# Kernel optimization log

Measured on AMD Instinct MI355X. Metric: run time of the kernel, lower is better.

## Reference

```python
import jax, jax.numpy as jnp
import numpy as np

NUM_HEADS = 16
HEAD_DIM = 64  # att_output_dim // num_heads = 1024 // 16


def setup_inputs() -> dict:
    key = jax.random.key(0)
    ks = jax.random.split(key, 7)
    B, S, D_IN, D_OUT = 4, 2048, 1024, 1024
    std = 1.0 / np.sqrt(D_IN)
    return {
        "ts10_input": jax.random.normal(ks[0], (B, S, D_IN), dtype=jnp.float32),
        "Wq": jax.random.uniform(ks[1], (D_IN, D_OUT), jnp.float32, -std, std),
        "bq": jax.random.uniform(ks[2], (D_OUT,), jnp.float32, -std, std),
        "Wk": jax.random.uniform(ks[3], (D_IN, D_OUT), jnp.float32, -std, std),
        "bk": jax.random.uniform(ks[4], (D_OUT,), jnp.float32, -std, std),
        "Wv": jax.random.uniform(ks[5], (D_IN, D_OUT), jnp.float32, -std, std),
        "bv": jax.random.uniform(ks[6], (D_OUT,), jnp.float32, -std, std),
        "mask": 1,
    }


def reference(ts10_input, Wq, bq, Wk, bk, Wv, bv, mask):
    B, S, _ = ts10_input.shape
    H, Dh = NUM_HEADS, HEAD_DIM

    def split_heads(x):  # (B,S,H*Dh) -> (B,H,S,Dh)
        return x.reshape(B, S, H, Dh).transpose(0, 2, 1, 3)

    q = split_heads(ts10_input @ Wq + bq)
    k = split_heads(ts10_input @ Wk + bk)
    v = split_heads(ts10_input @ Wv + bv)

    scores = jnp.einsum("bhqd,bhkd->bhqk", q, k) / jnp.sqrt(jnp.float32(Dh))
    if mask:
        causal = jnp.tril(jnp.ones((S, S), dtype=bool))  # keep lower triangle incl diag
        scores = jnp.where(causal, scores, -jnp.inf)
    probs = jax.nn.softmax(scores, axis=-1)
    ctx = jnp.einsum("bhqk,bhkd->bhqd", probs, v)
    return ctx.transpose(0, 2, 1, 3).reshape(B, S, H * Dh)
```

## Files before the change

kernel.cpp:

```cpp
#include <hip/hip_runtime.h>

typedef __bf16 bf16x8 __attribute__((ext_vector_type(8)));
typedef __bf16 bf16x4 __attribute__((ext_vector_type(4)));
typedef short s16x4 __attribute__((ext_vector_type(4)));
typedef float f32x4 __attribute__((ext_vector_type(4)));
typedef unsigned short u16x8 __attribute__((ext_vector_type(8)));
typedef unsigned short u16x4 __attribute__((ext_vector_type(4)));
typedef unsigned int u32x2 __attribute__((ext_vector_type(2)));
typedef unsigned int __attribute__((address_space(1))) as1_uint;
typedef unsigned int __attribute__((address_space(3))) as3_uint;

#define S_LEN 2048
#define NB 4
#define NH 16
#define HD 64
#define DM 1024

#define Q_SCALE 0.18033688011112042f

__device__ __forceinline__ unsigned short f2bf(float f) {
  union { float f; unsigned int u; } v; v.f = f;
  unsigned int r = v.u + 0x7fffu + ((v.u >> 16) & 1u);
  return (unsigned short)(r >> 16);
}

__device__ __forceinline__ unsigned int fbits(float f) {
  union { float f; unsigned int u; } v; v.f = f;
  return v.u;
}

__device__ __forceinline__ f32x4 mfma16(u16x4 a, u16x4 b, f32x4 c) {
#if __has_builtin(__builtin_amdgcn_mfma_f32_16x16x16_bf16)
  return __builtin_amdgcn_mfma_f32_16x16x16_bf16(
      __builtin_bit_cast(bf16x4, a), __builtin_bit_cast(bf16x4, b), c, 0, 0, 0);
#else
  return __builtin_amdgcn_mfma_f32_16x16x16bf16_1k(
      __builtin_bit_cast(s16x4, a), __builtin_bit_cast(s16x4, b), c, 0, 0, 0);
#endif
}

__global__ __launch_bounds__(256) void cvt_x(const float* __restrict__ x,
                                             unsigned short* __restrict__ xb) {
  int i = (blockIdx.x * 256 + threadIdx.x) * 8;
  f32x4 a = *(const f32x4*)(x + i);
  f32x4 b = *(const f32x4*)(x + i + 4);
  u16x8 o;
  o[0] = f2bf(a[0]); o[1] = f2bf(a[1]); o[2] = f2bf(a[2]); o[3] = f2bf(a[3]);
  o[4] = f2bf(b[0]); o[5] = f2bf(b[1]); o[6] = f2bf(b[2]); o[7] = f2bf(b[3]);
  *(u16x8*)(xb + i) = o;
}

__global__ __launch_bounds__(256) void cvt_wt(const float* __restrict__ Wq,
                                              const float* __restrict__ Wk,
                                              const float* __restrict__ Wv,
                                              unsigned short* __restrict__ wt) {
  const float* W = (blockIdx.z == 0) ? Wq : (blockIdx.z == 1) ? Wk : Wv;
  unsigned short* WT = wt + (size_t)blockIdx.z * DM * DM;
  __shared__ float tile[32][33];
  int tx = threadIdx.x & 31, ty = threadIdx.x >> 5;
  int k0 = blockIdx.x * 32, n0 = blockIdx.y * 32;
#pragma unroll
  for (int i = 0; i < 4; ++i)
    tile[ty + 8 * i][tx] = W[(size_t)(k0 + ty + 8 * i) * DM + n0 + tx];
  __syncthreads();
#pragma unroll
  for (int i = 0; i < 4; ++i)
    WT[(size_t)(n0 + ty + 8 * i) * DM + k0 + tx] = f2bf(tile[tx][ty + 8 * i]);
}

#define QKV_LDS_BYTES 147456
__global__ __launch_bounds__(512, 2) void qkv_gemm(const unsigned short* __restrict__ xb,
                                                   const unsigned short* __restrict__ wt,
                                                   const float* __restrict__ bq,
                                                   const float* __restrict__ bk,
                                                   const float* __restrict__ bv,
                                                   unsigned short* __restrict__ qo,
                                                   unsigned short* __restrict__ ko,
                                                   unsigned short* __restrict__ vto) {
  extern __shared__ char smem_dyn[];
  unsigned short* As = (unsigned short*)smem_dyn;
  unsigned short* Bs = As + 3 * 256 * 64;
  const int z = blockIdx.z;
  const unsigned short* WT = wt + (size_t)z * DM * DM;
  const float* bias = (z == 0) ? bq : (z == 1) ? bk : bv;
  const int m0 = blockIdx.x * 256;
  const int n0 = blockIdx.y * 128;
  const int tid = threadIdx.x;
  const int wave = tid >> 6, lane = tid & 63, quad = lane >> 4, lw = lane & 15;
  const int wm = (wave >> 1) * 64, wn = (wave & 1) * 64;

  f32x4 acc[4][4];
#pragma unroll
  for (int mt = 0; mt < 4; ++mt)
#pragma unroll
    for (int nt = 0; nt < 4; ++nt) acc[mt][nt] = (f32x4){0.f, 0.f, 0.f, 0.f};

  auto stage = [&](int tile) {
    const int kt = tile * 64;
    const int bsel = tile % 3;
    unsigned short* Ad = As + bsel * (256 * 64);
    unsigned short* Bd = Bs + bsel * (128 * 64);
#pragma unroll
    for (int i = 0; i < 4; ++i) {
      int c = i * 512 + tid;
      int row = c >> 3, scn = (c & 7) ^ (row & 7);
      __builtin_amdgcn_global_load_lds((const as1_uint*)(xb + (size_t)(m0 + row) * DM + kt + scn * 8),
                                       (as3_uint*)(Ad + c * 8), 16, 0, 0);
    }
#pragma unroll
    for (int i = 0; i < 2; ++i) {
      int c = i * 512 + tid;
      int row = c >> 3, scn = (c & 7) ^ (row & 7);
      __builtin_amdgcn_global_load_lds((const as1_uint*)(WT + (size_t)(n0 + row) * DM + kt + scn * 8),
                                       (as3_uint*)(Bd + c * 8), 16, 0, 0);
    }
  };

  stage(0);
  stage(1);
  asm volatile("s_waitcnt vmcnt(6)" ::: "memory");
  __builtin_amdgcn_s_barrier();
  asm volatile("" ::: "memory");

#pragma unroll
  for (int t = 0; t < 16; ++t) {
    if (t + 2 < 16) stage(t + 2);

    const unsigned short* Ab = As + (t % 3) * (256 * 64);
    const unsigned short* Bb = Bs + (t % 3) * (128 * 64);
    bf16x8 af[2][4], bfq[2][4];
#pragma unroll
    for (int k = 0; k < 2; ++k) {
#pragma unroll
      for (int mt = 0; mt < 4; ++mt) {
        int r = wm + mt * 16 + lw;
        af[k][mt] = *(const bf16x8*)(Ab + r * 64 + (((k * 4 + quad) ^ (r & 7)) * 8));
      }
#pragma unroll
      for (int nt = 0; nt < 4; ++nt) {
        int r = wn + nt * 16 + lw;
        bfq[k][nt] = *(const bf16x8*)(Bb + r * 64 + (((k * 4 + quad) ^ (r & 7)) * 8));
      }
    }
#pragma unroll
    for (int k = 0; k < 2; ++k)
#pragma unroll
      for (int mt = 0; mt < 4; ++mt)
#pragma unroll
        for (int nt = 0; nt < 4; ++nt)
          acc[mt][nt] = __builtin_amdgcn_mfma_f32_16x16x32_bf16(af[k][mt], bfq[k][nt], acc[mt][nt], 0, 0, 0);

    if (t < 15) {
      if (t < 14) asm volatile("s_waitcnt vmcnt(6)" ::: "memory");
      else        asm volatile("s_waitcnt vmcnt(0)" ::: "memory");
      __builtin_amdgcn_s_barrier();
      asm volatile("" ::: "memory");
    }
  }

  float bias4[4];
#pragma unroll
  for (int nt = 0; nt < 4; ++nt) bias4[nt] = bias[n0 + wn + nt * 16 + lw];

  if (z < 2) {
    unsigned short* dst = (z == 0) ? qo : ko;
    const float sc = (z == 0) ? Q_SCALE : 1.0f;
#pragma unroll
    for (int mt = 0; mt < 4; ++mt) {
#pragma unroll
      for (int nt = 0; nt < 4; ++nt) {
        int n = n0 + wn + nt * 16 + lw;
        int h = n >> 6, d = n & 63;
#pragma unroll
        for (int r = 0; r < 4; ++r) {
          int m = m0 + wm + mt * 16 + quad * 4 + r;
          int b = m >> 11, s = m & 2047;
          dst[((size_t)(b * NH + h) * S_LEN + s) * HD + d] = f2bf((acc[mt][nt][r] + bias4[nt]) * sc);
        }
      }
    }
  } else {
#pragma unroll
    for (int mt = 0; mt < 4; ++mt) {
#pragma unroll
      for (int nt = 0; nt < 4; ++nt) {
        int n = n0 + wn + nt * 16 + lw;
        int h = n >> 6, d = n & 63;
        int mb = m0 + wm + mt * 16 + quad * 4;
        int b = mb >> 11, s = mb & 2047;
        u16x4 pk;
#pragma unroll
        for (int r = 0; r < 4; ++r) pk[r] = f2bf(acc[mt][nt][r] + bias4[nt]);
        *(u16x4*)(vto + ((size_t)(b * NH + h) * HD + d) * S_LEN + s) = pk;
      }
    }
  }
}

__global__ __launch_bounds__(256, 4) void attn(const unsigned short* __restrict__ Qb,
                                               const unsigned short* __restrict__ Kb,
                                               const unsigned short* __restrict__ Vtb,
                                               float* __restrict__ out) {
  const int flat = blockIdx.x;
  const int bh_lo = flat & 7;
  const int qpair = (flat >> 3) & 15;
  const int bh_hi = flat >> 7;
  const int bh = bh_lo + 8 * bh_hi;
  const int b = bh >> 4, h = bh & 15;
  const int tid = threadIdx.x;
  const int wave = tid >> 6, lane = tid & 63;
  const int quad = lane >> 4, lw = lane & 15;
  const int qlo = qpair * 64;
  const int qhi = (31 - qpair) * 64;
  const unsigned short* Qp = Qb + (size_t)bh * S_LEN * HD;
  const unsigned short* Kp = Kb + (size_t)bh * S_LEN * HD;
  const unsigned short* Vp = Vtb + (size_t)bh * HD * S_LEN;

  __shared__ __align__(16) unsigned short Kl[2][64 * 64];
  __shared__ __align__(16) unsigned short Vl[2][64 * 64];

  bf16x8 aq[2][2];
#pragma unroll
  for (int rg = 0; rg < 2; ++rg) {
    const int qbase = rg ? qhi : qlo;
#pragma unroll
    for (int kc = 0; kc < 2; ++kc)
      aq[rg][kc] = *(const bf16x8*)(Qp + (size_t)(qbase + wave * 16 + lw) * HD + kc * 32 + quad * 8);
  }

  u16x4 ones4;
#pragma unroll
  for (int i = 0; i < 4; ++i) ones4[i] = 0x3F80;

  f32x4 accO[2][4];
  f32x4 accL[2];
#pragma unroll
  for (int rg = 0; rg < 2; ++rg) {
    accL[rg] = (f32x4){0.f, 0.f, 0.f, 0.f};
#pragma unroll
    for (int dg = 0; dg < 4; ++dg) accO[rg][dg] = (f32x4){0.f, 0.f, 0.f, 0.f};
  }

  const int qr0 = qlo + wave * 16 + lw;
  const int qr1 = qhi + wave * 16 + lw;

  const int T = 32 - qpair;

  {
#pragma unroll
    for (int i = 0; i < 2; ++i) {
      int idx = i * 256 + tid;
      int r = idx >> 3, c = (idx & 7) ^ (r & 7);
      __builtin_amdgcn_global_load_lds((const as1_uint*)(Kp + (size_t)r * HD + c * 8),
                                       (as3_uint*)(Kl[0] + idx * 8), 16, 0, 0);
      __builtin_amdgcn_global_load_lds((const as1_uint*)(Vp + (size_t)r * S_LEN + c * 8),
                                       (as3_uint*)(Vl[0] + idx * 8), 16, 0, 0);
    }
  }

  for (int t = 0; t < T; ++t) {
    const int kv = t * 64;
    const int cur = t & 1;
    __syncthreads();

    if (t + 1 < T) {
      const int kvn = kv + 64;
#pragma unroll
      for (int i = 0; i < 2; ++i) {
        int idx = i * 256 + tid;
        int r = idx >> 3, c = (idx & 7) ^ (r & 7);
        __builtin_amdgcn_global_load_lds((const as1_uint*)(Kp + (size_t)(kvn + r) * HD + c * 8),
                                         (as3_uint*)(Kl[cur ^ 1] + idx * 8), 16, 0, 0);
        __builtin_amdgcn_global_load_lds((const as1_uint*)(Vp + (size_t)r * S_LEN + kvn + c * 8),
                                         (as3_uint*)(Vl[cur ^ 1] + idx * 8), 16, 0, 0);
      }
    }

    const bool a0 = (t <= qpair);
    const bool d0 = (t == qpair);
    const bool d1 = (t == T - 1);

#pragma unroll
    for (int g = 0; g < 4; ++g) {
      const unsigned short* kp = Kl[cur] + (g * 16 + lw) * 64;
      const int sw = lw & 7;
      bf16x8 kf0 = *(const bf16x8*)(kp + ((quad ^ sw) * 8));
      bf16x8 kf1 = *(const bf16x8*)(kp + (((4 + quad) ^ sw) * 8));

      u16x4 pf[2];
#pragma unroll
      for (int rg = 0; rg < 2; ++rg) {
        if (rg == 0 && !a0) continue;
        f32x4 s = (f32x4){0.f, 0.f, 0.f, 0.f};
        s = __builtin_amdgcn_mfma_f32_16x16x32_bf16(kf0, aq[rg][0], s, 0, 0, 0);
        s = __builtin_amdgcn_mfma_f32_16x16x32_bf16(kf1, aq[rg][1], s, 0, 0, 0);
        const bool dg_ = rg ? d1 : d0;
        const int qr = rg ? qr1 : qr0;
        if (dg_) {
#pragma unroll
          for (int r = 0; r < 4; ++r) {
            float e = __builtin_amdgcn_exp2f(s[r]);
            s[r] = (kv + g * 16 + quad * 4 + r > qr) ? 0.f : e;
          }
        } else {
#pragma unroll
          for (int r = 0; r < 4; ++r) s[r] = __builtin_amdgcn_exp2f(s[r]);
        }
        u32x2 pk;
        pk[0] = (fbits(s[1]) & 0xFFFF0000u) | (fbits(s[0]) >> 16);
        pk[1] = (fbits(s[3]) & 0xFFFF0000u) | (fbits(s[2]) >> 16);
        pf[rg] = __builtin_bit_cast(u16x4, pk);
      }

#pragma unroll
      for (int dg = 0; dg < 4; ++dg) {
        const int row = dg * 16 + lw;
        const int slot = (2 * g + (quad >> 1)) ^ (lw & 7);
        u16x4 vf = *(const u16x4*)(Vl[cur] + row * 64 + slot * 8 + (quad & 1) * 4);
        if (a0) accO[0][dg] = mfma16(pf[0], vf, accO[0][dg]);
        accO[1][dg] = mfma16(pf[1], vf, accO[1][dg]);
      }
      if (a0) accL[0] = mfma16(pf[0], ones4, accL[0]);
      accL[1] = mfma16(pf[1], ones4, accL[1]);
    }
  }

#pragma unroll
  for (int rg = 0; rg < 2; ++rg) {
    const int qbase = rg ? qhi : qlo;
    float* op = out + ((size_t)b * S_LEN + qbase + wave * 16 + quad * 4) * DM + h * HD + lw;
#pragma unroll
    for (int r = 0; r < 4; ++r) {
      float inv = 1.0f / accL[rg][r];
#pragma unroll
      for (int dg = 0; dg < 4; ++dg) op[(size_t)r * DM + dg * 16] = accO[rg][dg][r] * inv;
    }
  }
}

extern "C" void kernel_launch(void* const* d_in, const int* in_sizes, int n_in,
                              void* d_out, int out_size, void* d_ws, size_t ws_size,
                              hipStream_t stream) {
  const float* x = (const float*)d_in[0];
  const float* Wq = (const float*)d_in[1];
  const float* bq = (const float*)d_in[2];
  const float* Wk = (const float*)d_in[3];
  const float* bk = (const float*)d_in[4];
  const float* Wv = (const float*)d_in[5];
  const float* bv = (const float*)d_in[6];
  float* out = (float*)d_out;

  char* ws = (char*)d_ws;
  unsigned short* xb = (unsigned short*)(ws + 0);
  unsigned short* wt = (unsigned short*)(ws + 16777216);
  unsigned short* qb = (unsigned short*)(ws + 23068672);
  unsigned short* kb = (unsigned short*)(ws + 39845888);
  unsigned short* vt = (unsigned short*)(ws + 56623104);

  hipFuncSetAttribute((const void*)qkv_gemm,
                      hipFuncAttributeMaxDynamicSharedMemorySize, QKV_LDS_BYTES);

  hipLaunchKernelGGL(cvt_x, dim3(4096), dim3(256), 0, stream, x, xb);
  hipLaunchKernelGGL(cvt_wt, dim3(32, 32, 3), dim3(256), 0, stream, Wq, Wk, Wv, wt);
  hipLaunchKernelGGL(qkv_gemm, dim3(32, 8, 3), dim3(512), QKV_LDS_BYTES, stream,
                     xb, wt, bq, bk, bv, qb, kb, vt);
  hipLaunchKernelGGL(attn, dim3(1024), dim3(256), 0, stream, qb, kb, vt, out);
}
```

Baseline: 221.9 us.

## Split attention into one q-tile per block, read V directly, fuse convert kernels

Merges the x and weight conversion kernels into a single launch, which removes one kernel launch. The attention kernel no longer pairs low and high query tiles. It now runs one 64-row query tile per block, with 2048 blocks ordered longest-first and occupancy raised to 6. V is no longer staged through LDS and is read directly from global memory per MFMA, which halves the LDS footprint. A setprio hint is added around the compute. The uncoalesced strided global V reads and the loss of the paired load balancing could offset the gains from higher occupancy.

```diff
diff --git a/kernel.cpp b/kernel.cpp
--- a/kernel.cpp
+++ b/kernel.cpp
@@ -39,33 +39,38 @@
 #endif
 }
 
-__global__ __launch_bounds__(256) void cvt_x(const float* __restrict__ x,
-                                             unsigned short* __restrict__ xb) {
-  int i = (blockIdx.x * 256 + threadIdx.x) * 8;
-  f32x4 a = *(const f32x4*)(x + i);
-  f32x4 b = *(const f32x4*)(x + i + 4);
-  u16x8 o;
-  o[0] = f2bf(a[0]); o[1] = f2bf(a[1]); o[2] = f2bf(a[2]); o[3] = f2bf(a[3]);
-  o[4] = f2bf(b[0]); o[5] = f2bf(b[1]); o[6] = f2bf(b[2]); o[7] = f2bf(b[3]);
-  *(u16x8*)(xb + i) = o;
-}
-
-__global__ __launch_bounds__(256) void cvt_wt(const float* __restrict__ Wq,
-                                              const float* __restrict__ Wk,
-                                              const float* __restrict__ Wv,
-                                              unsigned short* __restrict__ wt) {
-  const float* W = (blockIdx.z == 0) ? Wq : (blockIdx.z == 1) ? Wk : Wv;
-  unsigned short* WT = wt + (size_t)blockIdx.z * DM * DM;
+__global__ __launch_bounds__(256) void cvt_all(const float* __restrict__ x,
+                                               unsigned short* __restrict__ xb,
+                                               const float* __restrict__ Wq,
+                                               const float* __restrict__ Wk,
+                                               const float* __restrict__ Wv,
+                                               unsigned short* __restrict__ wt) {
   __shared__ float tile[32][33];
-  int tx = threadIdx.x & 31, ty = threadIdx.x >> 5;
-  int k0 = blockIdx.x * 32, n0 = blockIdx.y * 32;
-#pragma unroll
-  for (int i = 0; i < 4; ++i)
-    tile[ty + 8 * i][tx] = W[(size_t)(k0 + ty + 8 * i) * DM + n0 + tx];
-  __syncthreads();
-#pragma unroll
-  for (int i = 0; i < 4; ++i)
-    WT[(size_t)(n0 + ty + 8 * i) * DM + k0 + tx] = f2bf(tile[tx][ty + 8 * i]);
+  const int bid = blockIdx.x;
+  if (bid < 4096) {
+    int i = (bid * 256 + threadIdx.x) * 8;
+    f32x4 a = *(const f32x4*)(x + i);
+    f32x4 b = *(const f32x4*)(x + i + 4);
+    u16x8 o;
+    o[0] = f2bf(a[0]); o[1] = f2bf(a[1]); o[2] = f2bf(a[2]); o[3] = f2bf(a[3]);
+    o[4] = f2bf(b[0]); o[5] = f2bf(b[1]); o[6] = f2bf(b[2]); o[7] = f2bf(b[3]);
+    *(u16x8*)(xb + i) = o;
+  } else {
+    const int r = bid - 4096;
+    const int z = r >> 10;
+    const int rr = r & 1023;
+    const float* W = (z == 0) ? Wq : (z == 1) ? Wk : Wv;
+    unsigned short* WT = wt + (size_t)z * DM * DM;
+    int tx = threadIdx.x & 31, ty = threadIdx.x >> 5;
+    int k0 = (rr & 31) * 32, n0 = (rr >> 5) * 32;
+#pragma unroll
+    for (int i = 0; i < 4; ++i)
+      tile[ty + 8 * i][tx] = W[(size_t)(k0 + ty + 8 * i) * DM + n0 + tx];
+    __syncthreads();
+#pragma unroll
+    for (int i = 0; i < 4; ++i)
+      WT[(size_t)(n0 + ty + 8 * i) * DM + k0 + tx] = f2bf(tile[tx][ty + 8 * i]);
+  }
 }
 
 #define QKV_LDS_BYTES 147456
@@ -197,65 +202,50 @@
   }
 }
 
-__global__ __launch_bounds__(256, 4) void attn(const unsigned short* __restrict__ Qb,
+__global__ __launch_bounds__(256, 6) void attn(const unsigned short* __restrict__ Qb,
                                                const unsigned short* __restrict__ Kb,
                                                const unsigned short* __restrict__ Vtb,
                                                float* __restrict__ out) {
   const int flat = blockIdx.x;
   const int bh_lo = flat & 7;
-  const int qpair = (flat >> 3) & 15;
-  const int bh_hi = flat >> 7;
-  const int bh = bh_lo + 8 * bh_hi;
+  const int rest = flat >> 3;
+  const int qidx = 31 - (rest >> 3);
+  const int bh_hi = rest & 7;
+  const int bh = bh_lo | (bh_hi << 3);
   const int b = bh >> 4, h = bh & 15;
   const int tid = threadIdx.x;
   const int wave = tid >> 6, lane = tid & 63;
   const int quad = lane >> 4, lw = lane & 15;
-  const int qlo = qpair * 64;
-  const int qhi = (31 - qpair) * 64;
   const unsigned short* Qp = Qb + (size_t)bh * S_LEN * HD;
   const unsigned short* Kp = Kb + (size_t)bh * S_LEN * HD;
   const unsigned short* Vp = Vtb + (size_t)bh * HD * S_LEN;
 
   __shared__ __align__(16) unsigned short Kl[2][64 * 64];
-  __shared__ __align__(16) unsigned short Vl[2][64 * 64];
-
-  bf16x8 aq[2][2];
-#pragma unroll
-  for (int rg = 0; rg < 2; ++rg) {
-    const int qbase = rg ? qhi : qlo;
-#pragma unroll
-    for (int kc = 0; kc < 2; ++kc)
-      aq[rg][kc] = *(const bf16x8*)(Qp + (size_t)(qbase + wave * 16 + lw) * HD + kc * 32 + quad * 8);
-  }
+
+  const int qbase = qidx * 64;
+  bf16x8 aq[2];
+#pragma unroll
+  for (int kc = 0; kc < 2; ++kc)
+    aq[kc] = *(const bf16x8*)(Qp + (size_t)(qbase + wave * 16 + lw) * HD + kc * 32 + quad * 8);
 
   u16x4 ones4;
 #pragma unroll
   for (int i = 0; i < 4; ++i) ones4[i] = 0x3F80;
 
-  f32x4 accO[2][4];
-  f32x4 accL[2];
-#pragma unroll
-  for (int rg = 0; rg < 2; ++rg) {
-    accL[rg] = (f32x4){0.f, 0.f, 0.f, 0.f};
-#pragma unroll
-    for (int dg = 0; dg < 4; ++dg) accO[rg][dg] = (f32x4){0.f, 0.f, 0.f, 0.f};
-  }
-
-  const int qr0 = qlo + wave * 16 + lw;
-  const int qr1 = qhi + wave * 16 + lw;
-
-  const int T = 32 - qpair;
-
-  {
-#pragma unroll
-    for (int i = 0; i < 2; ++i) {
-      int idx = i * 256 + tid;
-      int r = idx >> 3, c = (idx & 7) ^ (r & 7);
-      __builtin_amdgcn_global_load_lds((const as1_uint*)(Kp + (size_t)r * HD + c * 8),
-                                       (as3_uint*)(Kl[0] + idx * 8), 16, 0, 0);
-      __builtin_amdgcn_global_load_lds((const as1_uint*)(Vp + (size_t)r * S_LEN + c * 8),
-                                       (as3_uint*)(Vl[0] + idx * 8), 16, 0, 0);
-    }
+  f32x4 accO[4];
+  f32x4 accL = (f32x4){0.f, 0.f, 0.f, 0.f};
+#pragma unroll
+  for (int dg = 0; dg < 4; ++dg) accO[dg] = (f32x4){0.f, 0.f, 0.f, 0.f};
+
+  const int qr = qbase + wave * 16 + lw;
+  const int T = qidx + 1;
+
+#pragma unroll
+  for (int i = 0; i < 2; ++i) {
+    int idx = i * 256 + tid;
+    int r = idx >> 3, c = (idx & 7) ^ (r & 7);
+    __builtin_amdgcn_global_load_lds((const as1_uint*)(Kp + (size_t)r * HD + c * 8),
+                                     (as3_uint*)(Kl[0] + idx * 8), 16, 0, 0);
   }
 
   for (int t = 0; t < T; ++t) {
@@ -271,15 +261,11 @@
         int r = idx >> 3, c = (idx & 7) ^ (r & 7);
         __builtin_amdgcn_global_load_lds((const as1_uint*)(Kp + (size_t)(kvn + r) * HD + c * 8),
                                          (as3_uint*)(Kl[cur ^ 1] + idx * 8), 16, 0, 0);
-        __builtin_amdgcn_global_load_lds((const as1_uint*)(Vp + (size_t)r * S_LEN + kvn + c * 8),
-                                         (as3_uint*)(Vl[cur ^ 1] + idx * 8), 16, 0, 0);
-      }
-    }
-
-    const bool a0 = (t <= qpair);
-    const bool d0 = (t == qpair);
-    const bool d1 = (t == T - 1);
-
+      }
+    }
+
+    const bool diag = (t == qidx);
+    __builtin_amdgcn_s_setprio(1);
 #pragma unroll
     for (int g = 0; g < 4; ++g) {
       const unsigned short* kp = Kl[cur] + (g * 16 + lw) * 64;
@@ -287,54 +273,41 @@
       bf16x8 kf0 = *(const bf16x8*)(kp + ((quad ^ sw) * 8));
       bf16x8 kf1 = *(const bf16x8*)(kp + (((4 + quad) ^ sw) * 8));
 
-      u16x4 pf[2];
-#pragma unroll
-      for (int rg = 0; rg < 2; ++rg) {
-        if (rg == 0 && !a0) continue;
-        f32x4 s = (f32x4){0.f, 0.f, 0.f, 0.f};
-        s = __builtin_amdgcn_mfma_f32_16x16x32_bf16(kf0, aq[rg][0], s, 0, 0, 0);
-        s = __builtin_amdgcn_mfma_f32_16x16x32_bf16(kf1, aq[rg][1], s, 0, 0, 0);
-        const bool dg_ = rg ? d1 : d0;
-        const int qr = rg ? qr1 : qr0;
-        if (dg_) {
-#pragma unroll
-          for (int r = 0; r < 4; ++r) {
-            float e = __builtin_amdgcn_exp2f(s[r]);
-            s[r] = (kv + g * 16 + quad * 4 + r > qr) ? 0.f : e;
-          }
-        } else {
-#pragma unroll
-          for (int r = 0; r < 4; ++r) s[r] = __builtin_amdgcn_exp2f(s[r]);
+      f32x4 s = (f32x4){0.f, 0.f, 0.f, 0.f};
+      s = __builtin_amdgcn_mfma_f32_16x16x32_bf16(kf0, aq[0], s, 0, 0, 0);
+      s = __builtin_amdgcn_mfma_f32_16x16x32_bf16(kf1, aq[1], s, 0, 0, 0);
+      if (diag) {
+#pragma unroll
+        for (int r = 0; r < 4; ++r) {
+          float e = __builtin_amdgcn_exp2f(s[r]);
+          s[r] = (kv + g * 16 + quad * 4 + r > qr) ? 0.f : e;
         }
-        u32x2 pk;
-        pk[0] = (fbits(s[1]) & 0xFFFF0000u) | (fbits(s[0]) >> 16);
-        pk[1] = (fbits(s[3]) & 0xFFFF0000u) | (fbits(s[2]) >> 16);
-        pf[rg] = __builtin_bit_cast(u16x4, pk);
-      }
-
+      } else {
+#pragma unroll
+        for (int r = 0; r < 4; ++r) s[r] = __builtin_amdgcn_exp2f(s[r]);
+      }
+      u32x2 pk;
+      pk[0] = (fbits(s[1]) & 0xFFFF0000u) | (fbits(s[0]) >> 16);
+      pk[1] = (fbits(s[3]) & 0xFFFF0000u) | (fbits(s[2]) >> 16);
+      u16x4 pf = __builtin_bit_cast(u16x4, pk);
+
+      const unsigned short* vg = Vp + (size_t)lw * S_LEN + kv + g * 16 + quad * 4;
 #pragma unroll
       for (int dg = 0; dg < 4; ++dg) {
-        const int row = dg * 16 + lw;
-        const int slot = (2 * g + (quad >> 1)) ^ (lw & 7);
-        u16x4 vf = *(const u16x4*)(Vl[cur] + row * 64 + slot * 8 + (quad & 1) * 4);
-        if (a0) accO[0][dg] = mfma16(pf[0], vf, accO[0][dg]);
-        accO[1][dg] = mfma16(pf[1], vf, accO[1][dg]);
-      }
-      if (a0) accL[0] = mfma16(pf[0], ones4, accL[0]);
-      accL[1] = mfma16(pf[1], ones4, accL[1]);
-    }
-  }
-
-#pragma unroll
-  for (int rg = 0; rg < 2; ++rg) {
-    const int qbase = rg ? qhi : qlo;
-    float* op = out + ((size_t)b * S_LEN + qbase + wave * 16 + quad * 4) * DM + h * HD + lw;
-#pragma unroll
-    for (int r = 0; r < 4; ++r) {
-      float inv = 1.0f / accL[rg][r];
-#pragma unroll
-      for (int dg = 0; dg < 4; ++dg) op[(size_t)r * DM + dg * 16] = accO[rg][dg][r] * inv;
-    }
+        u16x4 vf = *(const u16x4*)(vg + (size_t)(dg * 16) * S_LEN);
+        accO[dg] = mfma16(pf, vf, accO[dg]);
+      }
+      accL = mfma16(pf, ones4, accL);
+    }
+    __builtin_amdgcn_s_setprio(0);
+  }
+
+  float* op = out + ((size_t)b * S_LEN + qbase + wave * 16 + quad * 4) * DM + h * HD + lw;
+#pragma unroll
+  for (int r = 0; r < 4; ++r) {
+    float inv = 1.0f / accL[r];
+#pragma unroll
+    for (int dg = 0; dg < 4; ++dg) op[(size_t)r * DM + dg * 16] = accO[dg][r] * inv;
   }
 }
 
@@ -360,9 +333,8 @@
   hipFuncSetAttribute((const void*)qkv_gemm,
                       hipFuncAttributeMaxDynamicSharedMemorySize, QKV_LDS_BYTES);
 
-  hipLaunchKernelGGL(cvt_x, dim3(4096), dim3(256), 0, stream, x, xb);
-  hipLaunchKernelGGL(cvt_wt, dim3(32, 32, 3), dim3(256), 0, stream, Wq, Wk, Wv, wt);
+  hipLaunchKernelGGL(cvt_all, dim3(7168), dim3(256), 0, stream, x, xb, Wq, Wk, Wv, wt);
   hipLaunchKernelGGL(qkv_gemm, dim3(32, 8, 3), dim3(512), QKV_LDS_BYTES, stream,
                      xb, wt, bq, bk, bv, qb, kb, vt);
-  hipLaunchKernelGGL(attn, dim3(1024), dim3(256), 0, stream, qb, kb, vt, out);
-}
+  hipLaunchKernelGGL(attn, dim3(2048), dim3(256), 0, stream, qb, kb, vt, out);
+}
```

After: 400.7 us. 80.6% more time.
